# Kernel tuning notes

Hardware: AMD Instinct MI355X
Metric: run time of the kernel (lower is better)

## Reference

```python
import jax, jax.numpy as jnp
import numpy as np
from jax import lax

B, T, N = 256, 2048, 64  # batch, max_seq_len, num_tags


def setup_inputs() -> dict:
    key = jax.random.key(0)
    k1, k2, k3 = jax.random.split(key, 3)
    x = jax.random.normal(k1, (B, T, N), dtype=jnp.float32)
    seq_len = jax.random.randint(k2, (B,), 1, T + 1).astype(jnp.int32)
    trans = (jax.random.normal(k3, (N, N), dtype=jnp.float32) * 0.1)
    return {"x": x, "seq_len": seq_len, "trans": trans}


def reference(x, seq_len, trans):
    # Viterbi decode (tfa.text.crf_decode): returns (tags [B,T] int32, scores [B] float)
    Bv, Tv, Nv = x.shape
    alpha0 = x[:, 0]                                   # [B,N]
    xs = jnp.swapaxes(x[:, 1:], 0, 1)                  # [T-1,B,N]
    valid = jnp.arange(1, Tv)[:, None] < seq_len[None, :]  # [T-1,B]
    ident = jnp.arange(Nv, dtype=jnp.int32)

    def fwd(alpha, inp):
        x_t, v = inp
        # scores[b, prev, cur] = alpha[b, prev] + trans[prev, cur]
        sc = alpha[:, :, None] + trans[None]           # [B,N,N]
        bp = jnp.argmax(sc, axis=1).astype(jnp.int32)  # [B,N] best prev tag per cur
        new_alpha = jnp.max(sc, axis=1) + x_t          # [B,N]
        # steps beyond seq_len: carry state, identity backpointer
        alpha_n = jnp.where(v[:, None], new_alpha, alpha)
        bp = jnp.where(v[:, None], bp, ident[None, :])
        return alpha_n, bp

    alpha_f, bps = lax.scan(fwd, alpha0, (xs, valid))  # bps: [T-1,B,N]
    scores = jnp.max(alpha_f, axis=-1)                 # [B]
    last = jnp.argmax(alpha_f, axis=-1).astype(jnp.int32)  # [B] tag at last step

    def bwd(tag, bp):
        prev = jnp.take_along_axis(bp, tag[:, None], axis=1)[:, 0]
        return prev, tag  # emit tag at step t+1, carry tag at step t

    first, rest = lax.scan(bwd, last, bps, reverse=True)   # rest: [T-1,B]
    tags = jnp.concatenate([first[:, None], jnp.swapaxes(rest, 0, 1)], axis=1)  # [B,T]
    return tags, scores
```

## Files before the change

### kernel.cpp

```cpp
#include <hip/hip_runtime.h>

#define BB 256
#define TT 2048
#define NN 64
#define CHK 512

template <int K>
__device__ __forceinline__ int dpp_ror_i(int v) {
  return __builtin_amdgcn_update_dpp(0, v, 0x120 | K, 0xF, 0xF, true);
}
template <int K>
__device__ __forceinline__ float dpp_ror_f(float v) {
  return __int_as_float(dpp_ror_i<K>(__float_as_int(v)));
}

__global__ __launch_bounds__(256, 1)
void crf_viterbi_kernel(const float* __restrict__ x,
                        const int* __restrict__ seq_len,
                        const float* __restrict__ trans,
                        float* __restrict__ out) {
  const int b = blockIdx.x;
  const int tid = threadIdx.x;
  const int lane = tid & 63;
  const int w = tid >> 6;
  const int c = lane & 15;
  const int jc = (w << 4) + c;

  __shared__ __align__(16) float alpha_s[2][NN];
  __shared__ unsigned char bp_s[(TT - 1) * NN];
  __shared__ int map_s[4][NN];

  const float* xb = x + (size_t)b * TT * NN;
  const int slen = seq_len[b];

  int idxv[16];
  idxv[0] = lane;
  idxv[1] = dpp_ror_i<1>(lane);   idxv[2] = dpp_ror_i<2>(lane);
  idxv[3] = dpp_ror_i<3>(lane);   idxv[4] = dpp_ror_i<4>(lane);
  idxv[5] = dpp_ror_i<5>(lane);   idxv[6] = dpp_ror_i<6>(lane);
  idxv[7] = dpp_ror_i<7>(lane);   idxv[8] = dpp_ror_i<8>(lane);
  idxv[9] = dpp_ror_i<9>(lane);   idxv[10] = dpp_ror_i<10>(lane);
  idxv[11] = dpp_ror_i<11>(lane); idxv[12] = dpp_ror_i<12>(lane);
  idxv[13] = dpp_ror_i<13>(lane); idxv[14] = dpp_ror_i<14>(lane);
  idxv[15] = dpp_ror_i<15>(lane);

  float tcv[16];
#pragma unroll
  for (int k = 0; k < 16; ++k) tcv[k] = trans[idxv[k] * NN + jc];

  if (w == 0) alpha_s[0][lane] = xb[lane];
  __syncthreads();

  float xn1 = xb[NN + jc];
  float xn2 = xb[2 * NN + jc];

  for (int t = 1; t < slen; ++t) {
    float xv = xn1;
    xn1 = xn2;
    {
      int tn = (t + 2 < TT) ? (t + 2) : (TT - 1);
      xn2 = xb[(size_t)tn * NN + jc];
    }
    const int pr = (t + 1) & 1;
    const int pw = t & 1;

    float av = alpha_s[pr][lane];

#define CAND(K) (dpp_ror_f<K>(av) + tcv[K])
#define LNK(K, mq, bq)                                       \
    {                                                        \
      float c_ = CAND(K);                                    \
      bool g_ = c_ > (mq);                                   \
      (mq) = g_ ? c_ : (mq);                                 \
      (bq) = g_ ? idxv[K] : (bq);                            \
    }
    float m0 = av + tcv[0]; int b0 = idxv[0];
    float m1 = CAND(4);     int b1 = idxv[4];
    float m2 = CAND(8);     int b2 = idxv[8];
    float m3 = CAND(12);    int b3 = idxv[12];
    LNK(1, m0, b0) LNK(5, m1, b1) LNK(9,  m2, b2) LNK(13, m3, b3)
    LNK(2, m0, b0) LNK(6, m1, b1) LNK(10, m2, b2) LNK(14, m3, b3)
    LNK(3, m0, b0) LNK(7, m1, b1) LNK(11, m2, b2) LNK(15, m3, b3)
    { bool g = m1 > m0; m0 = g ? m1 : m0; b0 = g ? b1 : b0; }
    { bool g = m3 > m2; m2 = g ? m3 : m2; b2 = g ? b3 : b2; }
    { bool g = m2 > m0; m0 = g ? m2 : m0; b0 = g ? b2 : b0; }
#undef LNK
#undef CAND

    {
      float pm = __shfl_xor(m0, 16, 64);
      int pb = __shfl_xor(b0, 16, 64);
      bool g = pm > m0; m0 = g ? pm : m0; b0 = g ? pb : b0;
    }
    {
      float pm = __shfl_xor(m0, 32, 64);
      int pb = __shfl_xor(b0, 32, 64);
      bool g = pm > m0; m0 = g ? pm : m0; b0 = g ? pb : b0;
    }

    if (lane < 16) {
      alpha_s[pw][jc] = m0 + xv;
      bp_s[(t - 1) * NN + jc] = (unsigned char)b0;
    }
    asm volatile("s_waitcnt lgkmcnt(0)\n\ts_barrier" ::: "memory");
  }

  const int pf = (slen - 1) & 1;
  float best = alpha_s[pf][lane];
  int last = lane;
#pragma unroll
  for (int mask = 1; mask < 64; mask <<= 1) {
    float ov = __shfl_xor(best, mask, 64);
    int oi = __shfl_xor(last, mask, 64);
    bool take = (ov > best) || (ov == best && oi < last);
    best = take ? ov : best;
    last = take ? oi : last;
  }
  const float lastf = (float)last;
  const int bTT = b * TT;

  for (int t = slen - 1 + tid; t < TT; t += 256) out[bTT + t] = lastf;
  if (tid == 0) out[BB * TT + b] = best;

  const int lo = CHK * w;
  const int hi = ((CHK * (w + 1) - 1) < (slen - 2)) ? (CHK * (w + 1) - 1)
                                                    : (slen - 2);
  {
    int s = lane;
    for (int r = hi; r >= lo; --r) s = bp_s[r * NN + s];
    map_s[w][lane] = s;
  }
  __syncthreads();

  const int e3 = last;
  const int e2 = map_s[3][e3];
  const int e1 = map_s[2][e2];
  const int e0 = map_s[1][e1];
  const int entry = (w == 3) ? e3 : (w == 2) ? e2 : (w == 1) ? e1 : e0;

  if (lane == 0) {
    int s = entry;
    for (int r = hi; r >= lo; --r) {
      s = bp_s[r * NN + s];
      out[bTT + r] = (float)s;
    }
  }
}

extern "C" void kernel_launch(void* const* d_in, const int* in_sizes, int n_in,
                              void* d_out, int out_size, void* d_ws, size_t ws_size,
                              hipStream_t stream) {
  const float* x = (const float*)d_in[0];
  const int* seq_len = (const int*)d_in[1];
  const float* trans = (const float*)d_in[2];
  float* out = (float*)d_out;

  crf_viterbi_kernel<<<BB, 256, 0, stream>>>(x, seq_len, trans, out);
}
```

Baseline: 792.9 us.

## Split argmax into max-then-index reduction using permlane swaps instead of shuffles

Replaces the fused value+index compare-select chain with a pure max tree over the 16 candidates, reduced across lanes with v_permlane16/32_swap instead of ds_bpermute-based shuffles. A second pass finds the smallest index whose candidate equals the max, also reduced via permlane swaps, which gives first-index argmax tie-breaking. This shortens the per-step serial dependency and avoids LDS-path shuffles, at the cost of extra compares and a second cross-lane reduction. It also skips the unused backtrack-map pass for wave 0.

Result: no change. 805.1 us (+1.5%).

```diff
diff --git a/kernel.cpp b/kernel.cpp
--- a/kernel.cpp
+++ b/kernel.cpp
@@ -12,6 +12,29 @@
 template <int K>
 __device__ __forceinline__ float dpp_ror_f(float v) {
   return __int_as_float(dpp_ror_i<K>(__float_as_int(v)));
+}
+
+__device__ __forceinline__ float rowpair_max(float m) {
+  int a = __float_as_int(m), b = a;
+  asm volatile("v_permlane16_swap_b32 %0, %1" : "+v"(a), "+v"(b));
+  float fa = __int_as_float(a), fb = __int_as_float(b);
+  return fmaxf(fa, fb);
+}
+__device__ __forceinline__ float half_max(float m) {
+  int a = __float_as_int(m), b = a;
+  asm volatile("v_permlane32_swap_b32 %0, %1" : "+v"(a), "+v"(b));
+  float fa = __int_as_float(a), fb = __int_as_float(b);
+  return fmaxf(fa, fb);
+}
+__device__ __forceinline__ int rowpair_min(int v) {
+  int a = v, b = v;
+  asm volatile("v_permlane16_swap_b32 %0, %1" : "+v"(a), "+v"(b));
+  return a < b ? a : b;
+}
+__device__ __forceinline__ int half_min(int v) {
+  int a = v, b = v;
+  asm volatile("v_permlane32_swap_b32 %0, %1" : "+v"(a), "+v"(b));
+  return a < b ? a : b;
 }
 
 __global__ __launch_bounds__(256, 1)
@@ -66,41 +89,56 @@
 
     float av = alpha_s[pr][lane];
 
-#define CAND(K) (dpp_ror_f<K>(av) + tcv[K])
-#define LNK(K, mq, bq)                                       \
-    {                                                        \
-      float c_ = CAND(K);                                    \
-      bool g_ = c_ > (mq);                                   \
-      (mq) = g_ ? c_ : (mq);                                 \
-      (bq) = g_ ? idxv[K] : (bq);                            \
-    }
-    float m0 = av + tcv[0]; int b0 = idxv[0];
-    float m1 = CAND(4);     int b1 = idxv[4];
-    float m2 = CAND(8);     int b2 = idxv[8];
-    float m3 = CAND(12);    int b3 = idxv[12];
-    LNK(1, m0, b0) LNK(5, m1, b1) LNK(9,  m2, b2) LNK(13, m3, b3)
-    LNK(2, m0, b0) LNK(6, m1, b1) LNK(10, m2, b2) LNK(14, m3, b3)
-    LNK(3, m0, b0) LNK(7, m1, b1) LNK(11, m2, b2) LNK(15, m3, b3)
-    { bool g = m1 > m0; m0 = g ? m1 : m0; b0 = g ? b1 : b0; }
-    { bool g = m3 > m2; m2 = g ? m3 : m2; b2 = g ? b3 : b2; }
-    { bool g = m2 > m0; m0 = g ? m2 : m0; b0 = g ? b2 : b0; }
-#undef LNK
-#undef CAND
+    float c0 = av + tcv[0];
+    float c1 = dpp_ror_f<1>(av) + tcv[1];
+    float c2 = dpp_ror_f<2>(av) + tcv[2];
+    float c3 = dpp_ror_f<3>(av) + tcv[3];
+    float c4 = dpp_ror_f<4>(av) + tcv[4];
+    float c5 = dpp_ror_f<5>(av) + tcv[5];
+    float c6 = dpp_ror_f<6>(av) + tcv[6];
+    float c7 = dpp_ror_f<7>(av) + tcv[7];
+    float c8 = dpp_ror_f<8>(av) + tcv[8];
+    float c9 = dpp_ror_f<9>(av) + tcv[9];
+    float c10 = dpp_ror_f<10>(av) + tcv[10];
+    float c11 = dpp_ror_f<11>(av) + tcv[11];
+    float c12 = dpp_ror_f<12>(av) + tcv[12];
+    float c13 = dpp_ror_f<13>(av) + tcv[13];
+    float c14 = dpp_ror_f<14>(av) + tcv[14];
+    float c15 = dpp_ror_f<15>(av) + tcv[15];
 
-    {
-      float pm = __shfl_xor(m0, 16, 64);
-      int pb = __shfl_xor(b0, 16, 64);
-      bool g = pm > m0; m0 = g ? pm : m0; b0 = g ? pb : b0;
-    }
-    {
-      float pm = __shfl_xor(m0, 32, 64);
-      int pb = __shfl_xor(b0, 32, 64);
-      bool g = pm > m0; m0 = g ? pm : m0; b0 = g ? pb : b0;
-    }
+    float m = fmaxf(fmaxf(fmaxf(fmaxf(c0, c1), fmaxf(c2, c3)),
+                          fmaxf(fmaxf(c4, c5), fmaxf(c6, c7))),
+                    fmaxf(fmaxf(fmaxf(c8, c9), fmaxf(c10, c11)),
+                          fmaxf(fmaxf(c12, c13), fmaxf(c14, c15))));
+    m = rowpair_max(m);
+    m = half_max(m);
+
+    int s0 = (c0 == m) ? idxv[0] : NN;
+    int s1 = (c1 == m) ? idxv[1] : NN;
+    int s2 = (c2 == m) ? idxv[2] : NN;
+    int s3 = (c3 == m) ? idxv[3] : NN;
+    int s4 = (c4 == m) ? idxv[4] : NN;
+    int s5 = (c5 == m) ? idxv[5] : NN;
+    int s6 = (c6 == m) ? idxv[6] : NN;
+    int s7 = (c7 == m) ? idxv[7] : NN;
+    int s8 = (c8 == m) ? idxv[8] : NN;
+    int s9 = (c9 == m) ? idxv[9] : NN;
+    int s10 = (c10 == m) ? idxv[10] : NN;
+    int s11 = (c11 == m) ? idxv[11] : NN;
+    int s12 = (c12 == m) ? idxv[12] : NN;
+    int s13 = (c13 == m) ? idxv[13] : NN;
+    int s14 = (c14 == m) ? idxv[14] : NN;
+    int s15 = (c15 == m) ? idxv[15] : NN;
+    int idx = min(min(min(min(s0, s1), min(s2, s3)),
+                      min(min(s4, s5), min(s6, s7))),
+                  min(min(min(s8, s9), min(s10, s11)),
+                      min(min(s12, s13), min(s14, s15))));
+    idx = rowpair_min(idx);
+    idx = half_min(idx);
 
     if (lane < 16) {
-      alpha_s[pw][jc] = m0 + xv;
-      bp_s[(t - 1) * NN + jc] = (unsigned char)b0;
+      alpha_s[pw][jc] = m + xv;
+      bp_s[(t - 1) * NN + jc] = (unsigned char)idx;
     }
     asm volatile("s_waitcnt lgkmcnt(0)\n\ts_barrier" ::: "memory");
   }
@@ -125,7 +163,7 @@
   const int lo = CHK * w;
   const int hi = ((CHK * (w + 1) - 1) < (slen - 2)) ? (CHK * (w + 1) - 1)
                                                     : (slen - 2);
-  {
+  if (w > 0) {
     int s = lane;
     for (int r = hi; r >= lo; --r) s = bp_s[r * NN + s];
     map_s[w][lane] = s;
```
